# Kernel tuning notes

Hardware: AMD Instinct MI355X
Metric: run time of the kernel (lower is better)

Reference implementation:

```python
import jax, jax.numpy as jnp
import numpy as np

N_USERS = 100000
N_ITEMS = 40000
DIM = 64
NNZ_UI = 1500000
NNZ_II = 1000000
NNZ_UU = 1500000
UI_LAYERS = 3
ITEM_LAYERS = 2
USER_LAYERS = 2
EPS = 1e-12


def spmm(rows, cols, vals, x, n_rows):
    # sparse COO matrix (rows, cols, vals) @ dense x -> [n_rows, d]
    return jax.ops.segment_sum(vals[:, None] * x[cols], rows, num_segments=n_rows)


def l2_normalize(x):
    # matches F.normalize(x, p=2, dim=1) with eps clamp
    n = jnp.linalg.norm(x, axis=1, keepdims=True)
    return x / jnp.maximum(n, EPS)


def setup_inputs() -> dict:
    key = jax.random.key(0)
    ks = jax.random.split(key, 13)
    N = N_USERS + N_ITEMS
    return {
        "user_ui_emb": jax.random.normal(ks[0], (N_USERS, DIM), jnp.float32) * 0.1,
        "item_ui_emb": jax.random.normal(ks[1], (N_ITEMS, DIM), jnp.float32) * 0.1,
        "uu_emb": jax.random.normal(ks[2], (N_USERS, DIM), jnp.float32) * 0.1,
        "ii_emb": jax.random.normal(ks[3], (N_ITEMS, DIM), jnp.float32) * 0.1,
        "ui_vals": jax.random.uniform(ks[4], (NNZ_UI,), jnp.float32) / 12.0,
        "ii_vals": jax.random.uniform(ks[5], (NNZ_II,), jnp.float32) / 25.0,
        "uu_vals": jax.random.uniform(ks[6], (NNZ_UU,), jnp.float32) / 15.0,
        "ui_rows": jax.random.randint(ks[7], (NNZ_UI,), 0, N, jnp.int32),
        "ui_cols": jax.random.randint(ks[8], (NNZ_UI,), 0, N, jnp.int32),
        "ii_rows": jax.random.randint(ks[9], (NNZ_II,), 0, N_ITEMS, jnp.int32),
        "ii_cols": jax.random.randint(ks[10], (NNZ_II,), 0, N_ITEMS, jnp.int32),
        "uu_rows": jax.random.randint(ks[11], (NNZ_UU,), 0, N_USERS, jnp.int32),
        "uu_cols": jax.random.randint(ks[12], (NNZ_UU,), 0, N_USERS, jnp.int32),
    }


def reference(user_ui_emb, item_ui_emb, uu_emb, ii_emb,
              ui_vals, ii_vals, uu_vals,
              ui_rows, ui_cols, ii_rows, ii_cols, uu_rows, uu_cols):
    N = N_USERS + N_ITEMS
    # II propagation (item_loss_ratio != 0)
    ii = ii_emb
    for _ in range(ITEM_LAYERS):
        ii = spmm(ii_rows, ii_cols, ii_vals, ii, N_ITEMS)
    # UU propagation (user_loss_ratio != 0)
    uu = uu_emb
    for _ in range(USER_LAYERS):
        uu = spmm(uu_rows, uu_cols, uu_vals, uu, N_USERS)
    # LightGCN UI propagation
    ego = jnp.concatenate([user_ui_emb, item_ui_emb], axis=0)  # [N, d]
    acc = ego
    for _ in range(UI_LAYERS):
        ego = spmm(ui_rows, ui_cols, ui_vals, ego, N)
        acc = acc + ego
    all_emb = acc / (UI_LAYERS + 1)  # mean over stacked layers
    u_ui_emb = all_emb[:N_USERS]
    i_ui_emb = all_emb[N_USERS:]
    i_ui_emb = i_ui_emb + l2_normalize(ii)
    u_ui_emb = u_ui_emb + l2_normalize(uu)
    return (u_ui_emb, i_ui_emb, ii, uu)
```

## Files before the change

kernel.cpp:

```cpp
#include <hip/hip_runtime.h>

#define N_USERS_C 100000
#define N_ITEMS_C 40000
#define NTOT_C    140000
#define DIM_C     64

__device__ __forceinline__ unsigned short f2bf(float f) {
    unsigned u = __float_as_uint(f);
    unsigned r = (u + 0x7FFFu + ((u >> 16) & 1u)) >> 16;
    return (unsigned short)r;
}


template <int LOG_BR>
__global__ __launch_bounds__(256) void bucket_hist(
    const int* __restrict__ rows, int row_off, int* __restrict__ bkt_count,
    int nnz, int NB) {
    __shared__ int cnt[256];
    if (threadIdx.x < NB) cnt[threadIdx.x] = 0;
    __syncthreads();
    for (int e = blockIdx.x * 256 + threadIdx.x; e < nnz; e += gridDim.x * 256)
        atomicAdd(&cnt[(rows[e] + row_off) >> LOG_BR], 1);
    __syncthreads();
    if (threadIdx.x < NB) {
        int c = cnt[threadIdx.x];
        if (c) atomicAdd(&bkt_count[threadIdx.x], c);
    }
}

__global__ __launch_bounds__(256) void bucket_scan(
    const int* __restrict__ bkt_count, int* __restrict__ bkt_start,
    int* __restrict__ bkt_cursor, int NB, int nnz) {
    __shared__ int s[256];
    int v = (threadIdx.x < NB) ? bkt_count[threadIdx.x] : 0;
    s[threadIdx.x] = v;
    __syncthreads();
    #pragma unroll
    for (int off = 1; off < 256; off <<= 1) {
        int t = (threadIdx.x >= off) ? s[threadIdx.x - off] : 0;
        __syncthreads();
        s[threadIdx.x] += t;
        __syncthreads();
    }
    if (threadIdx.x < NB) {
        int ex = s[threadIdx.x] - v;
        bkt_start[threadIdx.x] = ex;
        bkt_cursor[threadIdx.x] = ex;
    }
    if (threadIdx.x == 0) bkt_start[NB] = nnz;
}

template <int LOG_BR>
__global__ __launch_bounds__(256) void partition_edges(
    const int* __restrict__ rows, const int* __restrict__ cols,
    const float* __restrict__ vals, int row_off, int col_off,
    int* __restrict__ bkt_cursor, int2* __restrict__ inter, int nnz) {
    __shared__ int cnt[256];
    __shared__ int base[256];
    const int tile = blockIdx.x * 4096;
    cnt[threadIdx.x] = 0;
    __syncthreads();
    int myrow[16];
    #pragma unroll
    for (int i = 0; i < 16; ++i) {
        int e = tile + i * 256 + threadIdx.x;
        int r = (e < nnz) ? (rows[e] + row_off) : -1;
        myrow[i] = r;
        if (r >= 0) atomicAdd(&cnt[r >> LOG_BR], 1);
    }
    __syncthreads();
    {
        int c = cnt[threadIdx.x];
        if (c) base[threadIdx.x] = atomicAdd(&bkt_cursor[threadIdx.x], c);
        cnt[threadIdx.x] = 0;
    }
    __syncthreads();
    #pragma unroll
    for (int i = 0; i < 16; ++i) {
        int r = myrow[i];
        if (r < 0) continue;
        int b = r >> LOG_BR;
        int rank = atomicAdd(&cnt[b], 1);
        int e = tile + i * 256 + threadIdx.x;
        int rl = r & ((1 << LOG_BR) - 1);
        inter[base[b] + rank] = make_int2((rl << 18) | (cols[e] + col_off),
                                          __float_as_int(vals[e]));
    }
}

template <int LOG_BR>
__global__ __launch_bounds__(256) void bucket_to_csr(
    const int* __restrict__ bkt_start, const int2* __restrict__ inter,
    int2* __restrict__ spack, int* __restrict__ rowptr, int n_rows, int nnz) {
    const int BR = 1 << LOG_BR;
    const int C = BR / 256;
    __shared__ int hist[BR];
    __shared__ int bsum[256];
    const int b = blockIdx.x;
    const int lo = bkt_start[b], hi = bkt_start[b + 1];
    #pragma unroll
    for (int j = 0; j < C; ++j) hist[threadIdx.x * C + j] = 0;
    __syncthreads();
    for (int i = lo + threadIdx.x; i < hi; i += 256)
        atomicAdd(&hist[inter[i].x >> 18], 1);
    __syncthreads();
    int loc[4];
    int sum = 0;
    #pragma unroll
    for (int j = 0; j < C; ++j) { loc[j] = sum; sum += hist[threadIdx.x * C + j]; }
    bsum[threadIdx.x] = sum;
    __syncthreads();
    #pragma unroll
    for (int off = 1; off < 256; off <<= 1) {
        int t = (threadIdx.x >= off) ? bsum[threadIdx.x - off] : 0;
        __syncthreads();
        bsum[threadIdx.x] += t;
        __syncthreads();
    }
    int texcl = bsum[threadIdx.x] - sum;
    __syncthreads();
    #pragma unroll
    for (int j = 0; j < C; ++j) {
        int r = threadIdx.x * C + j;
        int abs0 = lo + texcl + loc[j];
        int grow = (b << LOG_BR) + r;
        if (grow < n_rows) rowptr[grow] = abs0;
        hist[r] = abs0;
    }
    if (b == gridDim.x - 1 && threadIdx.x == 0) rowptr[n_rows] = nnz;
    __syncthreads();
    for (int i = lo + threadIdx.x; i < hi; i += 256) {
        int2 p = inter[i];
        int pos = atomicAdd(&hist[p.x >> 18], 1);
        spack[pos] = make_int2(p.x & 0x3FFFF, p.y);
    }
}

__global__ __launch_bounds__(256) void concat2_to_bf16(
    const float* __restrict__ A, const float* __restrict__ B, int n4A,
    int n4tot, unsigned short* __restrict__ dst) {
    int gid = blockIdx.x * blockDim.x + threadIdx.x;
    if (gid >= n4tot) return;
    float4 v = (gid < n4A) ? ((const float4*)A)[gid] : ((const float4*)B)[gid - n4A];
    ushort4 o;
    o.x = f2bf(v.x); o.y = f2bf(v.y); o.z = f2bf(v.z); o.w = f2bf(v.w);
    ((ushort4*)dst)[gid] = o;
}

template <int MODE>
__global__ __launch_bounds__(256) void spmm_csr4(
    const int* __restrict__ rowptr, const int2* __restrict__ spack,
    const unsigned short* __restrict__ x, unsigned short* __restrict__ out_bf,
    float* __restrict__ out_f32, float* __restrict__ acc,
    const float* __restrict__ ego_u, const float* __restrict__ ego_i,
    int n_rows, int nnz) {
    const int wq   = (blockIdx.x * 256 + threadIdx.x) >> 6;
    const int lane = threadIdx.x & 63;
    const int l    = lane & 15;
    const int row  = wq * 4 + (lane >> 4);

    int j = rowptr[row];
    int e = rowptr[row + 1];
    int rem = e - j;
    int m1 = max(rem, __shfl_xor(rem, 16, 64));
    int mrem = max(m1, __shfl_xor(m1, 32, 64));

    const uint2* __restrict__ xq = (const uint2*)x;
    const int last = nnz - 1;

    float4 sa[4];
    #pragma unroll
    for (int u = 0; u < 4; ++u) sa[u] = make_float4(0.f, 0.f, 0.f, 0.f);

    if (mrem > 0) {
        int base = j;
        int2 p[4];
        #pragma unroll
        for (int u = 0; u < 4; ++u) p[u] = spack[min(base + u, last)];
        for (;;) {
            uint2 g[4];
            #pragma unroll
            for (int u = 0; u < 4; ++u)
                g[u] = xq[(u < rem) ? ((p[u].x << 4) + l) : l];
            int nb = base + 4;
            int2 q[4];
            #pragma unroll
            for (int u = 0; u < 4; ++u) q[u] = spack[min(nb + u, last)];
            #pragma unroll
            for (int u = 0; u < 4; ++u) {
                float v = (u < rem) ? __int_as_float(p[u].y) : 0.f;
                sa[u].x += v * __uint_as_float(g[u].x << 16);
                sa[u].y += v * __uint_as_float(g[u].x & 0xFFFF0000u);
                sa[u].z += v * __uint_as_float(g[u].y << 16);
                sa[u].w += v * __uint_as_float(g[u].y & 0xFFFF0000u);
            }
            mrem -= 4;
            if (mrem <= 0) break;
            rem -= 4;
            base = nb;
            #pragma unroll
            for (int u = 0; u < 4; ++u) p[u] = q[u];
        }
    }
    float4 s;
    s.x = (sa[0].x + sa[1].x) + (sa[2].x + sa[3].x);
    s.y = (sa[0].y + sa[1].y) + (sa[2].y + sa[3].y);
    s.z = (sa[0].z + sa[1].z) + (sa[2].z + sa[3].z);
    s.w = (sa[0].w + sa[1].w) + (sa[2].w + sa[3].w);

    const size_t idx4 = (size_t)row * 16 + l;
    if (MODE == 0 || MODE == 1 || MODE == 2) {
        ushort4 o;
        o.x = f2bf(s.x); o.y = f2bf(s.y); o.z = f2bf(s.z); o.w = f2bf(s.w);
        ((ushort4*)out_bf)[idx4] = o;
    }
    if (MODE == 1) {
        float4 e4 = (row < N_USERS_C)
            ? ((const float4*)ego_u)[idx4]
            : ((const float4*)ego_i)[(size_t)(row - N_USERS_C) * 16 + l];
        ((float4*)acc)[idx4] = make_float4(e4.x + s.x, e4.y + s.y,
                                           e4.z + s.z, e4.w + s.w);
    } else if (MODE == 2 || MODE == 3) {
        float4 a = ((const float4*)acc)[idx4];
        ((float4*)acc)[idx4] = make_float4(a.x + s.x, a.y + s.y,
                                           a.z + s.z, a.w + s.w);
    } else if (MODE == 4 || MODE == 5) {
        ((float4*)out_f32)[idx4] = s;
        float ss = s.x * s.x + s.y * s.y + s.z * s.z + s.w * s.w;
        #pragma unroll
        for (int off = 1; off < 16; off <<= 1) ss += __shfl_xor(ss, off, 64);
        float inv = 1.f / fmaxf(sqrtf(ss), 1e-12f);
        size_t aidx = idx4;
        if (MODE == 5) {
            int arow = (row < N_ITEMS_C) ? (N_USERS_C + row) : (row - N_ITEMS_C);
            aidx = (size_t)arow * 16 + l;
        }
        float4 a = ((const float4*)acc)[aidx];
        a.x = a.x * 0.25f + s.x * inv;
        a.y = a.y * 0.25f + s.y * inv;
        a.z = a.z * 0.25f + s.z * inv;
        a.w = a.w * 0.25f + s.w * inv;
        ((float4*)acc)[aidx] = a;
    }
}


template <int MODE>
static inline void run_spmm(const int* rowptr, const int2* spack,
                            const unsigned short* x, unsigned short* out_bf,
                            float* out_f32, float* acc, const float* ego_u,
                            const float* ego_i, int n_rows, int nnz, hipStream_t s) {
    spmm_csr4<MODE><<<n_rows / 16, 256, 0, s>>>(rowptr, spack, x, out_bf, out_f32,
                                                acc, ego_u, ego_i, n_rows, nnz);
}

extern "C" void kernel_launch(void* const* d_in, const int* in_sizes, int n_in,
                              void* d_out, int out_size, void* d_ws, size_t ws_size,
                              hipStream_t stream) {
    const float* user_ui = (const float*)d_in[0];
    const float* item_ui = (const float*)d_in[1];
    const float* uu_emb  = (const float*)d_in[2];
    const float* ii_emb  = (const float*)d_in[3];
    const float* ui_vals = (const float*)d_in[4];
    const float* ii_vals = (const float*)d_in[5];
    const float* uu_vals = (const float*)d_in[6];
    const int* ui_rows = (const int*)d_in[7];
    const int* ui_cols = (const int*)d_in[8];
    const int* ii_rows = (const int*)d_in[9];
    const int* ii_cols = (const int*)d_in[10];
    const int* uu_rows = (const int*)d_in[11];
    const int* uu_cols = (const int*)d_in[12];
    const int nnz_ui = in_sizes[4];
    const int nnz_ii = in_sizes[5];
    const int nnz_uu = in_sizes[6];
    const int nnz_cat = nnz_ii + nnz_uu;

    float* out    = (float*)d_out;
    float* acc    = out;
    float* acc_u  = acc;
    float* acc_i  = acc + (size_t)N_USERS_C * DIM_C;
    float* out_ii = out + (size_t)NTOT_C * DIM_C;
    float* out_uu = out_ii + (size_t)N_ITEMS_C * DIM_C;
    float* out_cat = out_ii;

    const size_t buf_bytes = (size_t)NTOT_C * DIM_C * sizeof(unsigned short);
    const size_t sp_ui  = (size_t)nnz_ui * sizeof(int2);
    const size_t sp_cat = (size_t)nnz_cat * sizeof(int2);
    const size_t meta_bytes = ((size_t)(NTOT_C + 1) + 1024) * sizeof(int);

    size_t slotA = sp_cat > sp_ui ? sp_cat : sp_ui;
    size_t slotB = slotA > buf_bytes ? slotA : buf_bytes;
    bool use_cat = ws_size >= slotA + slotB + buf_bytes + meta_bytes;
    if (!use_cat) {
        size_t mx = sp_ui;
        if ((size_t)nnz_ii * sizeof(int2) > mx) mx = (size_t)nnz_ii * sizeof(int2);
        if ((size_t)nnz_uu * sizeof(int2) > mx) mx = (size_t)nnz_uu * sizeof(int2);
        slotA = mx;
        slotB = buf_bytes;
    }

    char* p = (char*)d_ws;
    int2* spack = (int2*)p;                     p += slotA;
    int2* inter = (int2*)p;
    unsigned short* buf0 = (unsigned short*)p;  p += slotB;
    unsigned short* buf1 = (unsigned short*)p;  p += buf_bytes;
    int* rowptr     = (int*)p;
    int* bkt_count  = rowptr + (NTOT_C + 1);
    int* bkt_start  = bkt_count + 257;
    int* bkt_cursor = bkt_start + 258;

    const int n4tot = NTOT_C * DIM_C / 4;
    const int n4u   = N_USERS_C * DIM_C / 4;
    const int n4i   = N_ITEMS_C * DIM_C / 4;

    {
        const int NB = (NTOT_C + 1023) >> 10;
        hipMemsetAsync(bkt_count, 0, (size_t)NB * sizeof(int), stream);
        bucket_hist<10><<<512, 256, 0, stream>>>(ui_rows, 0, bkt_count, nnz_ui, NB);
        bucket_scan<<<1, 256, 0, stream>>>(bkt_count, bkt_start, bkt_cursor, NB, nnz_ui);
        partition_edges<10><<<(nnz_ui + 4095) / 4096, 256, 0, stream>>>(
            ui_rows, ui_cols, ui_vals, 0, 0, bkt_cursor, inter, nnz_ui);
        bucket_to_csr<10><<<NB, 256, 0, stream>>>(bkt_start, inter, spack, rowptr,
                                                  NTOT_C, nnz_ui);
    }
    concat2_to_bf16<<<(n4tot + 255) / 256, 256, 0, stream>>>(user_ui, item_ui,
                                                             n4u, n4tot, buf1);
    run_spmm<1>(rowptr, spack, buf1, buf0, nullptr, acc, user_ui, item_ui,
                NTOT_C, nnz_ui, stream);
    run_spmm<2>(rowptr, spack, buf0, buf1, nullptr, acc, nullptr, nullptr,
                NTOT_C, nnz_ui, stream);
    run_spmm<3>(rowptr, spack, buf1, nullptr, nullptr, acc, nullptr, nullptr,
                NTOT_C, nnz_ui, stream);

    if (use_cat) {
        const int NB = (NTOT_C + 1023) >> 10;
        hipMemsetAsync(bkt_count, 0, (size_t)NB * sizeof(int), stream);
        bucket_hist<10><<<512, 256, 0, stream>>>(ii_rows, 0, bkt_count, nnz_ii, NB);
        bucket_hist<10><<<512, 256, 0, stream>>>(uu_rows, N_ITEMS_C, bkt_count,
                                                 nnz_uu, NB);
        bucket_scan<<<1, 256, 0, stream>>>(bkt_count, bkt_start, bkt_cursor, NB,
                                           nnz_cat);
        partition_edges<10><<<(nnz_ii + 4095) / 4096, 256, 0, stream>>>(
            ii_rows, ii_cols, ii_vals, 0, 0, bkt_cursor, inter, nnz_ii);
        partition_edges<10><<<(nnz_uu + 4095) / 4096, 256, 0, stream>>>(
            uu_rows, uu_cols, uu_vals, N_ITEMS_C, N_ITEMS_C, bkt_cursor, inter,
            nnz_uu);
        bucket_to_csr<10><<<NB, 256, 0, stream>>>(bkt_start, inter, spack, rowptr,
                                                  NTOT_C, nnz_cat);
        concat2_to_bf16<<<(n4tot + 255) / 256, 256, 0, stream>>>(ii_emb, uu_emb,
                                                                 n4i, n4tot, buf1);
        run_spmm<0>(rowptr, spack, buf1, buf0, nullptr, nullptr, nullptr, nullptr,
                    NTOT_C, nnz_cat, stream);
        run_spmm<5>(rowptr, spack, buf0, nullptr, out_cat, acc, nullptr, nullptr,
                    NTOT_C, nnz_cat, stream);
    } else {
        {
            const int NB = (N_ITEMS_C + 255) >> 8;
            hipMemsetAsync(bkt_count, 0, (size_t)NB * sizeof(int), stream);
            bucket_hist<8><<<512, 256, 0, stream>>>(ii_rows, 0, bkt_count, nnz_ii, NB);
            bucket_scan<<<1, 256, 0, stream>>>(bkt_count, bkt_start, bkt_cursor,
                                               NB, nnz_ii);
            partition_edges<8><<<(nnz_ii + 4095) / 4096, 256, 0, stream>>>(
                ii_rows, ii_cols, ii_vals, 0, 0, bkt_cursor, inter, nnz_ii);
            bucket_to_csr<8><<<NB, 256, 0, stream>>>(bkt_start, inter, spack,
                                                     rowptr, N_ITEMS_C, nnz_ii);
        }
        concat2_to_bf16<<<(n4i + 255) / 256, 256, 0, stream>>>(ii_emb, ii_emb,
                                                               n4i, n4i, buf0);
        run_spmm<0>(rowptr, spack, buf0, buf1, nullptr, nullptr, nullptr, nullptr,
                    N_ITEMS_C, nnz_ii, stream);
        run_spmm<4>(rowptr, spack, buf1, nullptr, out_ii, acc_i, nullptr, nullptr,
                    N_ITEMS_C, nnz_ii, stream);
        {
            const int NB = (N_USERS_C + 511) >> 9;
            hipMemsetAsync(bkt_count, 0, (size_t)NB * sizeof(int), stream);
            bucket_hist<9><<<512, 256, 0, stream>>>(uu_rows, 0, bkt_count, nnz_uu, NB);
            bucket_scan<<<1, 256, 0, stream>>>(bkt_count, bkt_start, bkt_cursor,
                                               NB, nnz_uu);
            partition_edges<9><<<(nnz_uu + 4095) / 4096, 256, 0, stream>>>(
                uu_rows, uu_cols, uu_vals, 0, 0, bkt_cursor, inter, nnz_uu);
            bucket_to_csr<9><<<NB, 256, 0, stream>>>(bkt_start, inter, spack,
                                                     rowptr, N_USERS_C, nnz_uu);
        }
        concat2_to_bf16<<<(n4u + 255) / 256, 256, 0, stream>>>(uu_emb, uu_emb,
                                                               n4u, n4u, buf0);
        run_spmm<0>(rowptr, spack, buf0, buf1, nullptr, nullptr, nullptr, nullptr,
                    N_USERS_C, nnz_uu, stream);
        run_spmm<4>(rowptr, spack, buf1, nullptr, out_uu, acc_u, nullptr, nullptr,
                    N_USERS_C, nnz_uu, stream);
    }
}
```

Measured before the change: 641.1 us.

## Replace bucketed two-pass COO-to-CSR build with per-row histogram, scan, atomic scatter

Replaces the bucket histogram, bucket partition and per-bucket CSR sort with a direct per-row atomic histogram, a three-kernel hierarchical prefix scan, and a direct atomic-cursor scatter into the packed CSR array. This removes the intermediate edge buffer and one full pass over the edges. In exchange it uses global atomics on per-row counters and scatters writes randomly. Edge order within a row becomes nondeterministic, so float summation order can change between runs.

```diff
diff --git a/kernel.cpp b/kernel.cpp
--- a/kernel.cpp
+++ b/kernel.cpp
@@ -4,6 +4,7 @@
 #define N_ITEMS_C 40000
 #define NTOT_C    140000
 #define DIM_C     64
+#define CDIV(a, b) (((a) + (b) - 1) / (b))
 
 __device__ __forceinline__ unsigned short f2bf(float f) {
     unsigned u = __float_as_uint(f);
@@ -12,128 +13,74 @@
 }
 
 
-template <int LOG_BR>
-__global__ __launch_bounds__(256) void bucket_hist(
-    const int* __restrict__ rows, int row_off, int* __restrict__ bkt_count,
-    int nnz, int NB) {
-    __shared__ int cnt[256];
-    if (threadIdx.x < NB) cnt[threadIdx.x] = 0;
+__global__ __launch_bounds__(256) void row_hist(
+    const int* __restrict__ rows, int row_off, int* __restrict__ cnt, int nnz) {
+    int i = blockIdx.x * 256 + threadIdx.x;
+    if (i < nnz) atomicAdd(&cnt[rows[i] + row_off], 1);
+}
+
+__global__ __launch_bounds__(256) void scan_blk(
+    const int* __restrict__ cnt, int* __restrict__ rowptr,
+    int* __restrict__ bsum, int n) {
+    __shared__ int s[256];
+    const int i0 = blockIdx.x * 1024 + threadIdx.x * 4;
+    int v0 = (i0 + 0 < n) ? cnt[i0 + 0] : 0;
+    int v1 = (i0 + 1 < n) ? cnt[i0 + 1] : 0;
+    int v2 = (i0 + 2 < n) ? cnt[i0 + 2] : 0;
+    int v3 = (i0 + 3 < n) ? cnt[i0 + 3] : 0;
+    int t = v0 + v1 + v2 + v3;
+    s[threadIdx.x] = t;
     __syncthreads();
-    for (int e = blockIdx.x * 256 + threadIdx.x; e < nnz; e += gridDim.x * 256)
-        atomicAdd(&cnt[(rows[e] + row_off) >> LOG_BR], 1);
-    __syncthreads();
-    if (threadIdx.x < NB) {
-        int c = cnt[threadIdx.x];
-        if (c) atomicAdd(&bkt_count[threadIdx.x], c);
-    }
-}
-
-__global__ __launch_bounds__(256) void bucket_scan(
-    const int* __restrict__ bkt_count, int* __restrict__ bkt_start,
-    int* __restrict__ bkt_cursor, int NB, int nnz) {
+    #pragma unroll
+    for (int off = 1; off < 256; off <<= 1) {
+        int u = (threadIdx.x >= off) ? s[threadIdx.x - off] : 0;
+        __syncthreads();
+        s[threadIdx.x] += u;
+        __syncthreads();
+    }
+    int ex = s[threadIdx.x] - t;
+    if (i0 + 0 < n) rowptr[i0 + 0] = ex;
+    if (i0 + 1 < n) rowptr[i0 + 1] = ex + v0;
+    if (i0 + 2 < n) rowptr[i0 + 2] = ex + v0 + v1;
+    if (i0 + 3 < n) rowptr[i0 + 3] = ex + v0 + v1 + v2;
+    if (threadIdx.x == 255) bsum[blockIdx.x] = s[255];
+}
+
+__global__ __launch_bounds__(256) void scan_top(int* __restrict__ bsum, int nb) {
     __shared__ int s[256];
-    int v = (threadIdx.x < NB) ? bkt_count[threadIdx.x] : 0;
+    int v = (threadIdx.x < nb) ? bsum[threadIdx.x] : 0;
     s[threadIdx.x] = v;
     __syncthreads();
     #pragma unroll
     for (int off = 1; off < 256; off <<= 1) {
-        int t = (threadIdx.x >= off) ? s[threadIdx.x - off] : 0;
+        int u = (threadIdx.x >= off) ? s[threadIdx.x - off] : 0;
         __syncthreads();
-        s[threadIdx.x] += t;
+        s[threadIdx.x] += u;
         __syncthreads();
     }
-    if (threadIdx.x < NB) {
-        int ex = s[threadIdx.x] - v;
-        bkt_start[threadIdx.x] = ex;
-        bkt_cursor[threadIdx.x] = ex;
-    }
-    if (threadIdx.x == 0) bkt_start[NB] = nnz;
-}
-
-template <int LOG_BR>
-__global__ __launch_bounds__(256) void partition_edges(
+    if (threadIdx.x < nb) bsum[threadIdx.x] = s[threadIdx.x] - v;
+}
+
+__global__ __launch_bounds__(256) void scan_add(
+    int* __restrict__ rowptr, const int* __restrict__ bsum,
+    int* __restrict__ cursor, int n, int nnz) {
+    int i = blockIdx.x * 256 + threadIdx.x;
+    if (i < n) {
+        int v = rowptr[i] + bsum[i >> 10];
+        rowptr[i] = v;
+        cursor[i] = v;
+    }
+    if (i == 0) rowptr[n] = nnz;
+}
+
+__global__ __launch_bounds__(256) void direct_scatter(
     const int* __restrict__ rows, const int* __restrict__ cols,
     const float* __restrict__ vals, int row_off, int col_off,
-    int* __restrict__ bkt_cursor, int2* __restrict__ inter, int nnz) {
-    __shared__ int cnt[256];
-    __shared__ int base[256];
-    const int tile = blockIdx.x * 4096;
-    cnt[threadIdx.x] = 0;
-    __syncthreads();
-    int myrow[16];
-    #pragma unroll
-    for (int i = 0; i < 16; ++i) {
-        int e = tile + i * 256 + threadIdx.x;
-        int r = (e < nnz) ? (rows[e] + row_off) : -1;
-        myrow[i] = r;
-        if (r >= 0) atomicAdd(&cnt[r >> LOG_BR], 1);
-    }
-    __syncthreads();
-    {
-        int c = cnt[threadIdx.x];
-        if (c) base[threadIdx.x] = atomicAdd(&bkt_cursor[threadIdx.x], c);
-        cnt[threadIdx.x] = 0;
-    }
-    __syncthreads();
-    #pragma unroll
-    for (int i = 0; i < 16; ++i) {
-        int r = myrow[i];
-        if (r < 0) continue;
-        int b = r >> LOG_BR;
-        int rank = atomicAdd(&cnt[b], 1);
-        int e = tile + i * 256 + threadIdx.x;
-        int rl = r & ((1 << LOG_BR) - 1);
-        inter[base[b] + rank] = make_int2((rl << 18) | (cols[e] + col_off),
-                                          __float_as_int(vals[e]));
-    }
-}
-
-template <int LOG_BR>
-__global__ __launch_bounds__(256) void bucket_to_csr(
-    const int* __restrict__ bkt_start, const int2* __restrict__ inter,
-    int2* __restrict__ spack, int* __restrict__ rowptr, int n_rows, int nnz) {
-    const int BR = 1 << LOG_BR;
-    const int C = BR / 256;
-    __shared__ int hist[BR];
-    __shared__ int bsum[256];
-    const int b = blockIdx.x;
-    const int lo = bkt_start[b], hi = bkt_start[b + 1];
-    #pragma unroll
-    for (int j = 0; j < C; ++j) hist[threadIdx.x * C + j] = 0;
-    __syncthreads();
-    for (int i = lo + threadIdx.x; i < hi; i += 256)
-        atomicAdd(&hist[inter[i].x >> 18], 1);
-    __syncthreads();
-    int loc[4];
-    int sum = 0;
-    #pragma unroll
-    for (int j = 0; j < C; ++j) { loc[j] = sum; sum += hist[threadIdx.x * C + j]; }
-    bsum[threadIdx.x] = sum;
-    __syncthreads();
-    #pragma unroll
-    for (int off = 1; off < 256; off <<= 1) {
-        int t = (threadIdx.x >= off) ? bsum[threadIdx.x - off] : 0;
-        __syncthreads();
-        bsum[threadIdx.x] += t;
-        __syncthreads();
-    }
-    int texcl = bsum[threadIdx.x] - sum;
-    __syncthreads();
-    #pragma unroll
-    for (int j = 0; j < C; ++j) {
-        int r = threadIdx.x * C + j;
-        int abs0 = lo + texcl + loc[j];
-        int grow = (b << LOG_BR) + r;
-        if (grow < n_rows) rowptr[grow] = abs0;
-        hist[r] = abs0;
-    }
-    if (b == gridDim.x - 1 && threadIdx.x == 0) rowptr[n_rows] = nnz;
-    __syncthreads();
-    for (int i = lo + threadIdx.x; i < hi; i += 256) {
-        int2 p = inter[i];
-        int pos = atomicAdd(&hist[p.x >> 18], 1);
-        spack[pos] = make_int2(p.x & 0x3FFFF, p.y);
-    }
+    int* __restrict__ cursor, int2* __restrict__ spack, int nnz) {
+    int i = blockIdx.x * 256 + threadIdx.x;
+    if (i >= nnz) return;
+    int pos = atomicAdd(&cursor[rows[i] + row_off], 1);
+    spack[pos] = make_int2(cols[i] + col_off, __float_as_int(vals[i]));
 }
 
 __global__ __launch_bounds__(256) void concat2_to_bf16(
@@ -254,6 +201,14 @@
                                                 acc, ego_u, ego_i, n_rows, nnz);
 }
 
+static inline void build_scan(int* cnt, int* rowptr, int* bsum, int n_rows,
+                              int nnz, hipStream_t s) {
+    int nblk = CDIV(n_rows, 1024);
+    scan_blk<<<nblk, 256, 0, s>>>(cnt, rowptr, bsum, n_rows);
+    scan_top<<<1, 256, 0, s>>>(bsum, nblk);
+    scan_add<<<CDIV(n_rows, 256), 256, 0, s>>>(rowptr, bsum, cnt, n_rows, nnz);
+}
+
 extern "C" void kernel_launch(void* const* d_in, const int* in_sizes, int n_in,
                               void* d_out, int out_size, void* d_ws, size_t ws_size,
                               hipStream_t stream) {
@@ -285,46 +240,36 @@
 
     const size_t buf_bytes = (size_t)NTOT_C * DIM_C * sizeof(unsigned short);
     const size_t sp_ui  = (size_t)nnz_ui * sizeof(int2);
+    const size_t sp_ii  = (size_t)nnz_ii * sizeof(int2);
+    const size_t sp_uu  = (size_t)nnz_uu * sizeof(int2);
     const size_t sp_cat = (size_t)nnz_cat * sizeof(int2);
-    const size_t meta_bytes = ((size_t)(NTOT_C + 1) + 1024) * sizeof(int);
-
-    size_t slotA = sp_cat > sp_ui ? sp_cat : sp_ui;
-    size_t slotB = slotA > buf_bytes ? slotA : buf_bytes;
-    bool use_cat = ws_size >= slotA + slotB + buf_bytes + meta_bytes;
-    if (!use_cat) {
-        size_t mx = sp_ui;
-        if ((size_t)nnz_ii * sizeof(int2) > mx) mx = (size_t)nnz_ii * sizeof(int2);
-        if ((size_t)nnz_uu * sizeof(int2) > mx) mx = (size_t)nnz_uu * sizeof(int2);
-        slotA = mx;
-        slotB = buf_bytes;
-    }
+    const size_t meta_bytes = (size_t)(NTOT_C + 1 + 256) * sizeof(int);
+
+    size_t slot_sep = sp_ui > sp_ii ? (sp_ui > sp_uu ? sp_ui : sp_uu)
+                                    : (sp_ii > sp_uu ? sp_ii : sp_uu);
+    size_t slot_cat = sp_cat > sp_ui ? sp_cat : sp_ui;
+    bool use_cat = ws_size >= slot_cat + 2 * buf_bytes + meta_bytes;
+    size_t slotA = use_cat ? slot_cat : slot_sep;
 
     char* p = (char*)d_ws;
     int2* spack = (int2*)p;                     p += slotA;
-    int2* inter = (int2*)p;
-    unsigned short* buf0 = (unsigned short*)p;  p += slotB;
+    unsigned short* buf0 = (unsigned short*)p;
+    int* cnt = (int*)p;                         p += buf_bytes;
     unsigned short* buf1 = (unsigned short*)p;  p += buf_bytes;
-    int* rowptr     = (int*)p;
-    int* bkt_count  = rowptr + (NTOT_C + 1);
-    int* bkt_start  = bkt_count + 257;
-    int* bkt_cursor = bkt_start + 258;
+    int* rowptr = (int*)p;
+    int* bsum   = rowptr + (NTOT_C + 1);
 
     const int n4tot = NTOT_C * DIM_C / 4;
     const int n4u   = N_USERS_C * DIM_C / 4;
     const int n4i   = N_ITEMS_C * DIM_C / 4;
 
-    {
-        const int NB = (NTOT_C + 1023) >> 10;
-        hipMemsetAsync(bkt_count, 0, (size_t)NB * sizeof(int), stream);
-        bucket_hist<10><<<512, 256, 0, stream>>>(ui_rows, 0, bkt_count, nnz_ui, NB);
-        bucket_scan<<<1, 256, 0, stream>>>(bkt_count, bkt_start, bkt_cursor, NB, nnz_ui);
-        partition_edges<10><<<(nnz_ui + 4095) / 4096, 256, 0, stream>>>(
-            ui_rows, ui_cols, ui_vals, 0, 0, bkt_cursor, inter, nnz_ui);
-        bucket_to_csr<10><<<NB, 256, 0, stream>>>(bkt_start, inter, spack, rowptr,
-                                                  NTOT_C, nnz_ui);
-    }
-    concat2_to_bf16<<<(n4tot + 255) / 256, 256, 0, stream>>>(user_ui, item_ui,
-                                                             n4u, n4tot, buf1);
+    hipMemsetAsync(cnt, 0, (size_t)NTOT_C * sizeof(int), stream);
+    row_hist<<<CDIV(nnz_ui, 256), 256, 0, stream>>>(ui_rows, 0, cnt, nnz_ui);
+    build_scan(cnt, rowptr, bsum, NTOT_C, nnz_ui, stream);
+    direct_scatter<<<CDIV(nnz_ui, 256), 256, 0, stream>>>(
+        ui_rows, ui_cols, ui_vals, 0, 0, cnt, spack, nnz_ui);
+    concat2_to_bf16<<<CDIV(n4tot, 256), 256, 0, stream>>>(user_ui, item_ui,
+                                                          n4u, n4tot, buf1);
     run_spmm<1>(rowptr, spack, buf1, buf0, nullptr, acc, user_ui, item_ui,
                 NTOT_C, nnz_ui, stream);
     run_spmm<2>(rowptr, spack, buf0, buf1, nullptr, acc, nullptr, nullptr,
@@ -333,57 +278,40 @@
                 NTOT_C, nnz_ui, stream);
 
     if (use_cat) {
-        const int NB = (NTOT_C + 1023) >> 10;
-        hipMemsetAsync(bkt_count, 0, (size_t)NB * sizeof(int), stream);
-        bucket_hist<10><<<512, 256, 0, stream>>>(ii_rows, 0, bkt_count, nnz_ii, NB);
-        bucket_hist<10><<<512, 256, 0, stream>>>(uu_rows, N_ITEMS_C, bkt_count,
-                                                 nnz_uu, NB);
-        bucket_scan<<<1, 256, 0, stream>>>(bkt_count, bkt_start, bkt_cursor, NB,
-                                           nnz_cat);
-        partition_edges<10><<<(nnz_ii + 4095) / 4096, 256, 0, stream>>>(
-            ii_rows, ii_cols, ii_vals, 0, 0, bkt_cursor, inter, nnz_ii);
-        partition_edges<10><<<(nnz_uu + 4095) / 4096, 256, 0, stream>>>(
-            uu_rows, uu_cols, uu_vals, N_ITEMS_C, N_ITEMS_C, bkt_cursor, inter,
-            nnz_uu);
-        bucket_to_csr<10><<<NB, 256, 0, stream>>>(bkt_start, inter, spack, rowptr,
-                                                  NTOT_C, nnz_cat);
-        concat2_to_bf16<<<(n4tot + 255) / 256, 256, 0, stream>>>(ii_emb, uu_emb,
-                                                                 n4i, n4tot, buf1);
+        hipMemsetAsync(cnt, 0, (size_t)NTOT_C * sizeof(int), stream);
+        row_hist<<<CDIV(nnz_ii, 256), 256, 0, stream>>>(ii_rows, 0, cnt, nnz_ii);
+        row_hist<<<CDIV(nnz_uu, 256), 256, 0, stream>>>(uu_rows, N_ITEMS_C, cnt,
+                                                        nnz_uu);
+        build_scan(cnt, rowptr, bsum, NTOT_C, nnz_cat, stream);
+        direct_scatter<<<CDIV(nnz_ii, 256), 256, 0, stream>>>(
+            ii_rows, ii_cols, ii_vals, 0, 0, cnt, spack, nnz_ii);
+        direct_scatter<<<CDIV(nnz_uu, 256), 256, 0, stream>>>(
+            uu_rows, uu_cols, uu_vals, N_ITEMS_C, N_ITEMS_C, cnt, spack, nnz_uu);
+        concat2_to_bf16<<<CDIV(n4tot, 256), 256, 0, stream>>>(ii_emb, uu_emb,
+                                                              n4i, n4tot, buf1);
         run_spmm<0>(rowptr, spack, buf1, buf0, nullptr, nullptr, nullptr, nullptr,
                     NTOT_C, nnz_cat, stream);
         run_spmm<5>(rowptr, spack, buf0, nullptr, out_cat, acc, nullptr, nullptr,
                     NTOT_C, nnz_cat, stream);
     } else {
-        {
-            const int NB = (N_ITEMS_C + 255) >> 8;
-            hipMemsetAsync(bkt_count, 0, (size_t)NB * sizeof(int), stream);
-            bucket_hist<8><<<512, 256, 0, stream>>>(ii_rows, 0, bkt_count, nnz_ii, NB);
-            bucket_scan<<<1, 256, 0, stream>>>(bkt_count, bkt_start, bkt_cursor,
-                                               NB, nnz_ii);
-            partition_edges<8><<<(nnz_ii + 4095) / 4096, 256, 0, stream>>>(
-                ii_rows, ii_cols, ii_vals, 0, 0, bkt_cursor, inter, nnz_ii);
-            bucket_to_csr<8><<<NB, 256, 0, stream>>>(bkt_start, inter, spack,
-                                                     rowptr, N_ITEMS_C, nnz_ii);
-        }
-        concat2_to_bf16<<<(n4i + 255) / 256, 256, 0, stream>>>(ii_emb, ii_emb,
-                                                               n4i, n4i, buf0);
+        hipMemsetAsync(cnt, 0, (size_t)NTOT_C * sizeof(int), stream);
+        row_hist<<<CDIV(nnz_ii, 256), 256, 0, stream>>>(ii_rows, 0, cnt, nnz_ii);
+        build_scan(cnt, rowptr, bsum, N_ITEMS_C, nnz_ii, stream);
+        direct_scatter<<<CDIV(nnz_ii, 256), 256, 0, stream>>>(
+            ii_rows, ii_cols, ii_vals, 0, 0, cnt, spack, nnz_ii);
+        concat2_to_bf16<<<CDIV(n4i, 256), 256, 0, stream>>>(ii_emb, ii_emb,
+                                                            n4i, n4i, buf0);
         run_spmm<0>(rowptr, spack, buf0, buf1, nullptr, nullptr, nullptr, nullptr,
                     N_ITEMS_C, nnz_ii, stream);
         run_spmm<4>(rowptr, spack, buf1, nullptr, out_ii, acc_i, nullptr, nullptr,
                     N_ITEMS_C, nnz_ii, stream);
-        {
-            const int NB = (N_USERS_C + 511) >> 9;
-            hipMemsetAsync(bkt_count, 0, (size_t)NB * sizeof(int), stream);
-            bucket_hist<9><<<512, 256, 0, stream>>>(uu_rows, 0, bkt_count, nnz_uu, NB);
-            bucket_scan<<<1, 256, 0, stream>>>(bkt_count, bkt_start, bkt_cursor,
-                                               NB, nnz_uu);
-            partition_edges<9><<<(nnz_uu + 4095) / 4096, 256, 0, stream>>>(
-                uu_rows, uu_cols, uu_vals, 0, 0, bkt_cursor, inter, nnz_uu);
-            bucket_to_csr<9><<<NB, 256, 0, stream>>>(bkt_start, inter, spack,
-                                                     rowptr, N_USERS_C, nnz_uu);
-        }
-        concat2_to_bf16<<<(n4u + 255) / 256, 256, 0, stream>>>(uu_emb, uu_emb,
-                                                               n4u, n4u, buf0);
+        int* cnt2 = cnt + N_ITEMS_C;
+        row_hist<<<CDIV(nnz_uu, 256), 256, 0, stream>>>(uu_rows, 0, cnt2, nnz_uu);
+        build_scan(cnt2, rowptr, bsum, N_USERS_C, nnz_uu, stream);
+        direct_scatter<<<CDIV(nnz_uu, 256), 256, 0, stream>>>(
+            uu_rows, uu_cols, uu_vals, 0, 0, cnt2, spack, nnz_uu);
+        concat2_to_bf16<<<CDIV(n4u, 256), 256, 0, stream>>>(uu_emb, uu_emb,
+                                                            n4u, n4u, buf0);
         run_spmm<0>(rowptr, spack, buf0, buf1, nullptr, nullptr, nullptr, nullptr,
                     N_USERS_C, nnz_uu, stream);
         run_spmm<4>(rowptr, spack, buf1, nullptr, out_uu, acc_u, nullptr, nullptr,
```

After: 840.3 us. +31.1%, slower.
